# Performance work log

Measured on AMD Instinct MI355X. Metric: run time of the kernel, lower is better.

The kernel has to match this reference:

```python
import jax, jax.numpy as jnp
import numpy as np

N, E, G = 100000, 1600000, 64
FIN, D, OUT = 4, 64, 16
EPS = 1e-5


def _lin(key, fi, fo):
    kw, kb = jax.random.split(key)
    w = jax.random.normal(kw, (fi, fo), dtype=jnp.float32) / np.sqrt(fi)
    b = jnp.zeros((fo,), dtype=jnp.float32)
    return w, b


def setup_inputs() -> dict:
    key = jax.random.key(0)
    ks = jax.random.split(key, 24)
    inp = {}
    inp['h'] = jax.random.normal(ks[0], (N, FIN), dtype=jnp.float32)
    inp['pos'] = jax.random.normal(ks[1], (N, 3), dtype=jnp.float32)
    inp['edge_index'] = jax.random.randint(ks[2], (2, E), 0, N, dtype=jnp.int32)
    inp['batch'] = jnp.sort(jax.random.randint(ks[3], (N,), 0, G, dtype=jnp.int32))
    inp['fe_w'], inp['fe_b'] = _lin(ks[4], FIN, D)
    i = 5
    for c in ('c1', 'c2'):
        inp[c + 'h_w1'], inp[c + 'h_b1'] = _lin(ks[i], D, D); i += 1
        inp[c + 'h_w2'], inp[c + 'h_b2'] = _lin(ks[i], D, 3); i += 1
        inp[c + 'f_w1'], inp[c + 'f_b1'] = _lin(ks[i], D + 3, D); i += 1
        inp[c + 'f_w2'], inp[c + 'f_b2'] = _lin(ks[i], D, D); i += 1
        inp[c + 'g_w1'], inp[c + 'g_b1'] = _lin(ks[i], D, D); i += 1
        inp[c + 'g_gm'] = jnp.ones((D,), dtype=jnp.float32)
        inp[c + 'g_bt'] = jnp.zeros((D,), dtype=jnp.float32)
        inp[c + 'g_w2'], inp[c + 'g_b2'] = _lin(ks[i], D, D); i += 1
    inp['ro_w1'], inp['ro_b1'] = _lin(ks[i], D, D); i += 1
    inp['ro_w2'], inp['ro_b2'] = _lin(ks[i], D, OUT)
    return inp


def _mlp2(x, w1, b1, w2, b2):
    return jnp.maximum(x @ w1 + b1, 0.0) @ w2 + b2


def _bn(x, gm, bt):
    # BatchNorm1d in training mode: batch stats over the node axis
    m = jnp.mean(x, axis=0)
    v = jnp.var(x, axis=0)
    return (x - m) * jax.lax.rsqrt(v + EPS) * gm + bt


def _pointgnn_conv(x, pos, src, dst, hw1, hb1, hw2, hb2, fw1, fb1, fw2, fb2,
                   gw1, gb1, ggm, gbt, gw2, gb2):
    delta = _mlp2(x, hw1, hb1, hw2, hb2)                      # [N,3]
    rel = pos[src] - pos[dst] + delta[dst]                    # [E,3]
    msg = _mlp2(jnp.concatenate([rel, x[src]], axis=-1), fw1, fb1, fw2, fb2)  # [E,D]
    agg = jax.ops.segment_max(msg, dst, num_segments=x.shape[0])
    agg = jnp.where(jnp.isneginf(agg), 0.0, agg)              # empty segments -> 0
    g = jnp.maximum(agg @ gw1 + gb1, 0.0)
    g = _bn(g, ggm, gbt)
    return x + (g @ gw2 + gb2)


def reference(h, pos, edge_index, batch, fe_w, fe_b,
              c1h_w1, c1h_b1, c1h_w2, c1h_b2, c1f_w1, c1f_b1, c1f_w2, c1f_b2,
              c1g_w1, c1g_b1, c1g_gm, c1g_bt, c1g_w2, c1g_b2,
              c2h_w1, c2h_b1, c2h_w2, c2h_b2, c2f_w1, c2f_b1, c2f_w2, c2f_b2,
              c2g_w1, c2g_b1, c2g_gm, c2g_bt, c2g_w2, c2g_b2,
              ro_w1, ro_b1, ro_w2, ro_b2):
    src, dst = edge_index[0], edge_index[1]
    x = h @ fe_w + fe_b
    x = _pointgnn_conv(x, pos, src, dst, c1h_w1, c1h_b1, c1h_w2, c1h_b2,
                       c1f_w1, c1f_b1, c1f_w2, c1f_b2,
                       c1g_w1, c1g_b1, c1g_gm, c1g_bt, c1g_w2, c1g_b2)
    x = _pointgnn_conv(x, pos, src, dst, c2h_w1, c2h_b1, c2h_w2, c2h_b2,
                       c2f_w1, c2f_b1, c2f_w2, c2f_b2,
                       c2g_w1, c2g_b1, c2g_gm, c2g_bt, c2g_w2, c2g_b2)
    # global mean pool over graphs
    sums = jax.ops.segment_sum(x, batch, num_segments=G)
    cnts = jax.ops.segment_sum(jnp.ones((x.shape[0], 1), x.dtype), batch, num_segments=G)
    pooled = sums / jnp.maximum(cnts, 1.0)
    return _mlp2(pooled, ro_w1, ro_b1, ro_w2, ro_b2)
```

## Files before the change

kernel.cpp:

```cpp
#include <hip/hip_runtime.h>

#define NN 100000
#define NE 1600000
#define NG 64
#define EPS 1e-5f
#define SCAN_NB 98

#define FOR16(M) M(0) M(1) M(2) M(3) M(4) M(5) M(6) M(7) M(8) M(9) M(10) M(11) M(12) M(13) M(14) M(15)

#define WDECL(i) float4 wr##i##_;
#define LDW(i, RB, P) \
  wr##i##_.x = (P)[((RB) + 4 * i + 0) * 64 + lane]; \
  wr##i##_.y = (P)[((RB) + 4 * i + 1) * 64 + lane]; \
  wr##i##_.z = (P)[((RB) + 4 * i + 2) * 64 + lane]; \
  wr##i##_.w = (P)[((RB) + 4 * i + 3) * 64 + lane];
#define WPIN(i) asm volatile("" : "+v"(wr##i##_.x), "+v"(wr##i##_.y), "+v"(wr##i##_.z), "+v"(wr##i##_.w));
#define DOTR(i) { float4 v = xr[i]; \
  a0 = fmaf(v.x, wr##i##_.x, a0); a1 = fmaf(v.y, wr##i##_.y, a1); \
  a2 = fmaf(v.z, wr##i##_.z, a2); a3 = fmaf(v.w, wr##i##_.w, a3); }
#define DOTB(i, SRC) { \
  a0 = fmaf(bcast(SRC, 4 * i + 0), wr##i##_.x, a0); \
  a1 = fmaf(bcast(SRC, 4 * i + 1), wr##i##_.y, a1); \
  a2 = fmaf(bcast(SRC, 4 * i + 2), wr##i##_.z, a2); \
  a3 = fmaf(bcast(SRC, 4 * i + 3), wr##i##_.w, a3); }
#define DOTL(i) { float4 hv = hr[i]; \
  a0 = fmaf(hv.x, wr##i##_.x, a0); a1 = fmaf(hv.y, wr##i##_.y, a1); \
  a2 = fmaf(hv.z, wr##i##_.z, a2); a3 = fmaf(hv.w, wr##i##_.w, a3); }

#define BDECL(i) float4 br##i##_;
#define LDB(i, RB, P) \
  br##i##_.x = (P)[((RB) + 4 * i + 0) * 64 + lane]; \
  br##i##_.y = (P)[((RB) + 4 * i + 1) * 64 + lane]; \
  br##i##_.z = (P)[((RB) + 4 * i + 2) * 64 + lane]; \
  br##i##_.w = (P)[((RB) + 4 * i + 3) * 64 + lane];
#define BPIN(i) asm volatile("" : "+v"(br##i##_.x), "+v"(br##i##_.y), "+v"(br##i##_.z), "+v"(br##i##_.w));
#define DOTRB(i) { float4 v = xr[i]; \
  a0 = fmaf(v.x, br##i##_.x, a0); a1 = fmaf(v.y, br##i##_.y, a1); \
  a2 = fmaf(v.z, br##i##_.z, a2); a3 = fmaf(v.w, br##i##_.w, a3); }

__device__ __forceinline__ int wave_gid() {
  return __builtin_amdgcn_readfirstlane((int)((blockIdx.x * blockDim.x + threadIdx.x) >> 6));
}

__device__ __forceinline__ float bcast(float v, int l) {
  return __uint_as_float(__builtin_amdgcn_readlane(__float_as_uint(v), l));
}

__device__ __forceinline__ void graph_range(const int* __restrict__ batch, int g, int& s, int& e) {
  int a = 0, b = NN;
  while (a < b) { int m = (a + b) >> 1; if (batch[m] < g) a = m + 1; else b = m; }
  s = a;
  b = NN;
  while (a < b) { int m = (a + b) >> 1; if (batch[m] < g + 1) a = m + 1; else b = m; }
  e = a;
}

__global__ void k_zero(unsigned* __restrict__ hist, float* __restrict__ psum,
                       const float* __restrict__ pos, float4* __restrict__ pos4) {
  int i = blockIdx.x * blockDim.x + threadIdx.x;
  int st = gridDim.x * blockDim.x;
  for (int j = i; j < NN; j += st) {
    hist[j] = 0u;
    pos4[j] = make_float4(pos[(size_t)j * 3 + 0], pos[(size_t)j * 3 + 1],
                          pos[(size_t)j * 3 + 2], 0.f);
  }
  for (int j = i; j < NG * 64; j += st) psum[j] = 0.f;
}

__global__ void k_hist(const int* __restrict__ ei, unsigned* __restrict__ hist) {
  int i = blockIdx.x * blockDim.x + threadIdx.x;
  int st = gridDim.x * blockDim.x;
  for (int e = i; e < NE; e += st) atomicAdd(&hist[ei[NE + e]], 1u);
}

__global__ void k_scan1(const unsigned* __restrict__ hist, unsigned* __restrict__ coff,
                        unsigned* __restrict__ bsum) {
  __shared__ unsigned sd[256];
  int t = threadIdx.x;
  int base = blockIdx.x * 1024 + t * 4;
  unsigned v0 = (base + 0 < NN) ? hist[base + 0] : 0u;
  unsigned v1 = (base + 1 < NN) ? hist[base + 1] : 0u;
  unsigned v2 = (base + 2 < NN) ? hist[base + 2] : 0u;
  unsigned v3 = (base + 3 < NN) ? hist[base + 3] : 0u;
  unsigned tsum = v0 + v1 + v2 + v3;
  sd[t] = tsum;
  __syncthreads();
  for (int off = 1; off < 256; off <<= 1) {
    unsigned add = (t >= off) ? sd[t - off] : 0u;
    __syncthreads();
    sd[t] += add;
    __syncthreads();
  }
  unsigned p = sd[t] - tsum;
  if (t == 255) bsum[blockIdx.x] = sd[255];
  if (base + 0 < NN) coff[base + 0] = p; p += v0;
  if (base + 1 < NN) coff[base + 1] = p; p += v1;
  if (base + 2 < NN) coff[base + 2] = p; p += v2;
  if (base + 3 < NN) coff[base + 3] = p;
}

__global__ void k_scan2(unsigned* __restrict__ bsum) {
  __shared__ unsigned sd[128];
  int t = threadIdx.x;
  unsigned v = (t < SCAN_NB) ? bsum[t] : 0u;
  sd[t] = v;
  __syncthreads();
  for (int off = 1; off < 128; off <<= 1) {
    unsigned add = (t >= off) ? sd[t - off] : 0u;
    __syncthreads();
    sd[t] += add;
    __syncthreads();
  }
  if (t < SCAN_NB) bsum[t] = sd[t] - v;
}

__global__ void k_scan3(unsigned* __restrict__ coff, const unsigned* __restrict__ bsum,
                        unsigned* __restrict__ cursor) {
  int i = blockIdx.x * blockDim.x + threadIdx.x;
  if (i < NN) {
    unsigned v = coff[i] + bsum[i >> 10];
    coff[i] = v;
    cursor[i] = v;
  }
  if (i == 0) coff[NN] = NE;
}

__global__ void k_scatter(const int* __restrict__ ei, unsigned* __restrict__ cursor,
                          int* __restrict__ csrc) {
  int i = blockIdx.x * blockDim.x + threadIdx.x;
  int st = gridDim.x * blockDim.x;
  for (int e = i; e < NE; e += st) {
    int dst = ei[NE + e];
    unsigned p = atomicAdd(&cursor[dst], 1u);
    csrc[p] = ei[e];
  }
}

__global__ void __launch_bounds__(256) k_init_x(const float* __restrict__ h,
                                                const float* __restrict__ few,
                                                const float* __restrict__ feb,
                                                float* __restrict__ x) {
  int lane = threadIdx.x & 63;
  int wg = wave_gid();
  int nw = (gridDim.x * blockDim.x) >> 6;
  float c0 = few[0 * 64 + lane], c1 = few[1 * 64 + lane];
  float c2 = few[2 * 64 + lane], c3 = few[3 * 64 + lane];
  float b = feb[lane];
  for (int n = wg; n < NN; n += nw) {
    float4 hv = *(const float4*)(h + (size_t)n * 4);
    x[(size_t)n * 64 + lane] = fmaf(hv.x, c0, fmaf(hv.y, c1, fmaf(hv.z, c2, fmaf(hv.w, c3, b))));
  }
}

__global__ void __launch_bounds__(256) k_node_pre(
    const float* __restrict__ x, const float* __restrict__ pos,
    const float* __restrict__ hw1, const float* __restrict__ hb1,
    const float* __restrict__ hw2, const float* __restrict__ hb2,
    const float* __restrict__ fw1, const float* __restrict__ fb1,
    float* __restrict__ q, float* __restrict__ xa) {
  int lane = threadIdx.x & 63;
  int wg = wave_gid();
  int nw = (gridDim.x * blockDim.x) >> 6;
  FOR16(WDECL)
  FOR16(BDECL)
#define LD(i) LDW(i, 0, hw1)
  FOR16(LD)
#undef LD
#define LD(i) LDB(i, 3, fw1)
  FOR16(LD)
#undef LD
  FOR16(WPIN)
  FOR16(BPIN)
  float b1 = hb1[lane];
  float fb = fb1[lane];
  float u0 = hw2[lane * 3 + 0], u1 = hw2[lane * 3 + 1], u2 = hw2[lane * 3 + 2];
  float b20 = hb2[0], b21 = hb2[1], b22 = hb2[2];
  for (int n = wg; n < NN; n += nw) {
    const float4* xr = (const float4*)(x + (size_t)n * 64);
    float a0 = 0.f, a1 = 0.f, a2 = 0.f, a3 = 0.f;
    FOR16(DOTR)
    float t = fmaxf((a0 + a1) + (a2 + a3) + b1, 0.f);
    float p0 = t * u0, p1 = t * u1, p2 = t * u2;
#pragma unroll
    for (int off = 32; off; off >>= 1) {
      p0 += __shfl_xor(p0, off);
      p1 += __shfl_xor(p1, off);
      p2 += __shfl_xor(p2, off);
    }
    a0 = 0.f; a1 = 0.f; a2 = 0.f; a3 = 0.f;
    FOR16(DOTRB)
    xa[(size_t)n * 64 + lane] = (a0 + a1) + (a2 + a3) + fb;
    if (lane < 3) {
      float dc = (lane == 0) ? (p0 + b20) : ((lane == 1) ? (p1 + b21) : (p2 + b22));
      q[(size_t)n * 4 + lane] = pos[(size_t)n * 3 + lane] - dc;
    }
  }
}

__global__ void __launch_bounds__(256, 3) k_edge_csr(
    const float* __restrict__ xa, const float4* __restrict__ pos4,
    const float* __restrict__ q, const unsigned* __restrict__ coff,
    const int* __restrict__ csrc, const float* __restrict__ fw1,
    const float* __restrict__ fb2_, const float* __restrict__ fw2,
    float* __restrict__ agg) {
  __shared__ __align__(16) float hbuf[4][2][64];
  int lane = threadIdx.x & 63;
  int wid = threadIdx.x >> 6;
  int wg = wave_gid();
  int nw = (gridDim.x * blockDim.x) >> 6;
  FOR16(WDECL)
#define LD(i) LDW(i, 0, fw2)
  FOR16(LD)
#undef LD
  FOR16(WPIN)
  float pw0 = fw1[0 * 64 + lane], pw1 = fw1[1 * 64 + lane], pw2 = fw1[2 * 64 + lane];
  float bl = fb2_[lane];
  const float NEGINF = __int_as_float(0xff800000);
  for (int dst = wg; dst < NN; dst += nw) {
    unsigned s = coff[dst], e = coff[dst + 1];
    float mx;
    if (e > s) {
      float4 qd = *(const float4*)(q + (size_t)dst * 4);
      int src = csrc[s];
      float4 ps = pos4[src];
      float hh = xa[(size_t)src * 64 + lane];
      float pre = fmaxf(fmaf(ps.x - qd.x, pw0,
                        fmaf(ps.y - qd.y, pw1,
                        fmaf(ps.z - qd.z, pw2, hh))), 0.f);
      hbuf[wid][0][lane] = pre;
      int cur = 0;
      mx = NEGINF;
      for (unsigned i = s; i < e; ++i) {
        if (i + 1 < e) {
          int ns = csrc[i + 1];
          float4 ps2 = pos4[ns];
          float hh2 = xa[(size_t)ns * 64 + lane];
          float pre2 = fmaxf(fmaf(ps2.x - qd.x, pw0,
                             fmaf(ps2.y - qd.y, pw1,
                             fmaf(ps2.z - qd.z, pw2, hh2))), 0.f);
          hbuf[wid][cur ^ 1][lane] = pre2;
        }
        const float4* hr = (const float4*)hbuf[wid][cur];
        float a0 = bl, a1 = 0.f, a2 = 0.f, a3 = 0.f;
        DOTL(0) DOTL(1) DOTL(2) DOTL(3) DOTL(4) DOTL(5) DOTL(6) DOTL(7)
        __builtin_amdgcn_sched_barrier(0);
        DOTL(8) DOTL(9) DOTL(10) DOTL(11) DOTL(12) DOTL(13) DOTL(14) DOTL(15)
        mx = fmaxf(mx, (a0 + a1) + (a2 + a3));
        cur ^= 1;
      }
    } else {
      mx = 0.f;
    }
    agg[(size_t)dst * 64 + lane] = mx;
  }
}

__global__ void __launch_bounds__(256) k_g_bn(
    const float* __restrict__ agg, const float* __restrict__ gw1,
    const float* __restrict__ gb1, float* __restrict__ g, float* __restrict__ bnp) {
  __shared__ float2 red[4][64];
  int lane = threadIdx.x & 63;
  int wid = threadIdx.x >> 6;
  int wg = wave_gid();
  int nw = (gridDim.x * blockDim.x) >> 6;
  FOR16(WDECL)
#define LD(i) LDW(i, 0, gw1)
  FOR16(LD)
#undef LD
  FOR16(WPIN)
  float b = gb1[lane];
  float s = 0.f, ss = 0.f;
  for (int n = wg; n < NN; n += nw) {
    float av = agg[(size_t)n * 64 + lane];
    float a0 = 0.f, a1 = 0.f, a2 = 0.f, a3 = 0.f;
#define DB(i) DOTB(i, av)
    FOR16(DB)
#undef DB
    float gv = fmaxf((a0 + a1) + (a2 + a3) + b, 0.f);
    g[(size_t)n * 64 + lane] = gv;
    s += gv;
    ss += gv * gv;
  }
  red[wid][lane] = make_float2(s, ss);
  __syncthreads();
  if (wid == 0) {
    float2 r0 = red[0][lane], r1 = red[1][lane], r2 = red[2][lane], r3 = red[3][lane];
    bnp[(size_t)blockIdx.x * 128 + lane] = r0.x + r1.x + r2.x + r3.x;
    bnp[(size_t)blockIdx.x * 128 + 64 + lane] = r0.y + r1.y + r2.y + r3.y;
  }
}

#define NBLK_BN 256
__global__ void k_bn_final(const float* __restrict__ bnp, const float* __restrict__ gm,
                           const float* __restrict__ bt, const float* __restrict__ gw2,
                           const float* __restrict__ gb2, float* __restrict__ w2p,
                           float* __restrict__ b2p) {
  __shared__ float sums[128];
  __shared__ float sc[64], sh[64];
  int t = threadIdx.x;
  int c = t & 63;
  int kind = t >> 6;
  float acc = 0.f;
#pragma unroll 8
  for (int bId = 0; bId < NBLK_BN; ++bId) acc += bnp[(size_t)bId * 128 + kind * 64 + c];
  sums[t] = acc;
  __syncthreads();
  if (t < 64) {
    float mean = sums[t] * (1.f / (float)NN);
    float var = sums[64 + t] * (1.f / (float)NN) - mean * mean;
    float scale = gm[t] * rsqrtf(var + EPS);
    sc[t] = scale;
    sh[t] = bt[t] - mean * scale;
  }
  __syncthreads();
  for (int i = t; i < 4096; i += 128) {
    int d = i >> 6;
    w2p[i] = sc[d] * gw2[i];
  }
  if (t < 64) {
    float acc2 = gb2[t];
#pragma unroll 8
    for (int d = 0; d < 64; ++d) acc2 = fmaf(sh[d], gw2[d * 64 + t], acc2);
    b2p[t] = acc2;
  }
}

__global__ void __launch_bounds__(256) k_update(
    const float* __restrict__ g, const float* __restrict__ w2p,
    const float* __restrict__ b2p, float* __restrict__ x) {
  int lane = threadIdx.x & 63;
  int wg = wave_gid();
  int nw = (gridDim.x * blockDim.x) >> 6;
  FOR16(WDECL)
#define LD(i) LDW(i, 0, w2p)
  FOR16(LD)
#undef LD
  FOR16(WPIN)
  float b = b2p[lane];
  for (int n = wg; n < NN; n += nw) {
    const float4* xr = (const float4*)(g + (size_t)n * 64);
    float a0 = 0.f, a1 = 0.f, a2 = 0.f, a3 = 0.f;
    FOR16(DOTR)
    size_t idx = (size_t)n * 64 + lane;
    x[idx] = x[idx] + (a0 + a1) + (a2 + a3) + b;
  }
}

__global__ void __launch_bounds__(512) k_pool_partial(const float* __restrict__ x,
                                                      const int* __restrict__ batch,
                                                      float* __restrict__ psum) {
  __shared__ float red[8][64];
  int lane = threadIdx.x & 63;
  int wid = threadIdx.x >> 6;
  int g = blockIdx.x >> 2;
  int part = blockIdx.x & 3;
  int s, e;
  graph_range(batch, g, s, e);
  float acc = 0.f;
  for (int n = s + part * 8 + wid; n < e; n += 32) acc += x[(size_t)n * 64 + lane];
  red[wid][lane] = acc;
  __syncthreads();
  if (wid == 0) {
    float t = acc;
#pragma unroll
    for (int w = 1; w < 8; ++w) t += red[w][lane];
    atomicAdd(&psum[(size_t)g * 64 + lane], t);
  }
}

__global__ void __launch_bounds__(64) k_readout(
    const float* __restrict__ psum, const int* __restrict__ batch,
    const float* __restrict__ w1, const float* __restrict__ b1,
    const float* __restrict__ w2, const float* __restrict__ b2,
    float* __restrict__ out) {
  __shared__ float hs[64];
  int lane = threadIdx.x;
  int g = blockIdx.x;
  int s, e;
  graph_range(batch, g, s, e);
  float scale = 1.f / fmaxf((float)(e - s), 1.f);
  FOR16(WDECL)
#define LD(i) LDW(i, 0, w1)
  FOR16(LD)
#undef LD
  const float4* xr = (const float4*)(psum + (size_t)g * 64);
  float a0 = 0.f, a1 = 0.f, a2 = 0.f, a3 = 0.f;
  FOR16(DOTR)
  hs[lane] = fmaxf(((a0 + a1) + (a2 + a3)) * scale + b1[lane], 0.f);
  __syncthreads();
  if (lane < 16) {
    float acc = b2[lane];
#pragma unroll
    for (int l = 0; l < 64; ++l) acc = fmaf(hs[l], w2[l * 16 + lane], acc);
    out[(size_t)g * 16 + lane] = acc;
  }
}

extern "C" void kernel_launch(void* const* d_in, const int* in_sizes, int n_in,
                              void* d_out, int out_size, void* d_ws, size_t ws_size,
                              hipStream_t stream) {
  const float* h = (const float*)d_in[0];
  const float* pos = (const float*)d_in[1];
  const int* ei = (const int*)d_in[2];
  const int* batch = (const int*)d_in[3];
  const float* fe_w = (const float*)d_in[4];
  const float* fe_b = (const float*)d_in[5];
  const float* ro_w1 = (const float*)d_in[34];
  const float* ro_b1 = (const float*)d_in[35];
  const float* ro_w2 = (const float*)d_in[36];
  const float* ro_b2 = (const float*)d_in[37];
  float* out = (float*)d_out;

  char* ws = (char*)d_ws;
  const size_t SZ_ROW = (size_t)NN * 64 * sizeof(float);
  float* x = (float*)(ws); ws += SZ_ROW;
  float* xa = (float*)(ws); ws += SZ_ROW;
  float* agg = (float*)(ws); ws += SZ_ROW;
  float* q = (float*)(ws); ws += (size_t)NN * 4 * sizeof(float);
  float* bnp = (float*)(ws); ws += (size_t)NBLK_BN * 128 * sizeof(float);
  float* w2p = (float*)(ws); ws += 4096 * sizeof(float);
  float* b2p = (float*)(ws); ws += 256;
  float* psum = (float*)(ws); ws += (size_t)NG * 64 * sizeof(float);
  float4* pos4 = (float4*)(ws); ws += (size_t)NN * sizeof(float4);
  unsigned* cursor = (unsigned*)(ws); ws += ((size_t)NN * 4 + 256);
  unsigned* coff = (unsigned*)(ws); ws += ((size_t)(NN + 1) * 4 + 252);
  unsigned* bsum = (unsigned*)(ws); ws += 512;
  int* csrc = (int*)(ws); ws += (size_t)NE * 4;

  const int NB_NODE = 512;
  const int NB_EDGE = 4096;

  k_zero<<<256, 256, 0, stream>>>(cursor, psum, pos, pos4);
  k_hist<<<1024, 256, 0, stream>>>(ei, cursor);
  k_scan1<<<SCAN_NB, 256, 0, stream>>>(cursor, coff, bsum);
  k_scan2<<<1, 128, 0, stream>>>(bsum);
  k_scan3<<<392, 256, 0, stream>>>(coff, bsum, cursor);
  k_scatter<<<1024, 256, 0, stream>>>(ei, cursor, csrc);

  k_init_x<<<NB_NODE, 256, 0, stream>>>(h, fe_w, fe_b, x);

  for (int layer = 0; layer < 2; ++layer) {
    int base = (layer == 0) ? 6 : 20;
    const float* hw1 = (const float*)d_in[base + 0];
    const float* hb1 = (const float*)d_in[base + 1];
    const float* hw2 = (const float*)d_in[base + 2];
    const float* hb2 = (const float*)d_in[base + 3];
    const float* fw1 = (const float*)d_in[base + 4];
    const float* fb1 = (const float*)d_in[base + 5];
    const float* fw2 = (const float*)d_in[base + 6];
    const float* fb2 = (const float*)d_in[base + 7];
    const float* gw1 = (const float*)d_in[base + 8];
    const float* gb1 = (const float*)d_in[base + 9];
    const float* ggm = (const float*)d_in[base + 10];
    const float* gbt = (const float*)d_in[base + 11];
    const float* gw2 = (const float*)d_in[base + 12];
    const float* gb2 = (const float*)d_in[base + 13];

    k_node_pre<<<NB_NODE, 256, 0, stream>>>(x, pos, hw1, hb1, hw2, hb2, fw1, fb1, q, xa);
    k_edge_csr<<<NB_EDGE, 256, 0, stream>>>(xa, pos4, q, coff, csrc, fw1, fb2, fw2, agg);
    float* g = xa;
    k_g_bn<<<NBLK_BN, 256, 0, stream>>>(agg, gw1, gb1, g, bnp);
    k_bn_final<<<1, 128, 0, stream>>>(bnp, ggm, gbt, gw2, gb2, w2p, b2p);
    k_update<<<NB_NODE, 256, 0, stream>>>(g, w2p, b2p, x);
  }

  k_pool_partial<<<NG * 4, 512, 0, stream>>>(x, batch, psum);
  k_readout<<<NG, 64, 0, stream>>>(psum, batch, ro_w1, ro_b1, ro_w2, ro_b2, out);
}
```

Before: 1.434 ms.

## Use packed FMA with readlane broadcast in edge and g kernels

The edge kernel no longer stages the per-edge hidden vector in LDS double buffers. It now computes it in registers and broadcasts each element across lanes with readlane. Dot products in both the edge and g/BN kernels switch to two-wide packed FMAs (v_pk_fma_f32) on float2 accumulators, and the occupancy hint of 3 is dropped from the edge kernel's launch bounds. This removes LDS traffic and aims to double FMA throughput, but relies on 64 scalar readlanes per edge, which may serialize on the SALU/VALU path.

```diff
diff --git a/kernel.cpp b/kernel.cpp
--- a/kernel.cpp
+++ b/kernel.cpp
@@ -5,6 +5,8 @@
 #define NG 64
 #define EPS 1e-5f
 #define SCAN_NB 98
+
+typedef float v2f __attribute__((ext_vector_type(2)));
 
 #define FOR16(M) M(0) M(1) M(2) M(3) M(4) M(5) M(6) M(7) M(8) M(9) M(10) M(11) M(12) M(13) M(14) M(15)
 
@@ -18,14 +20,13 @@
 #define DOTR(i) { float4 v = xr[i]; \
   a0 = fmaf(v.x, wr##i##_.x, a0); a1 = fmaf(v.y, wr##i##_.y, a1); \
   a2 = fmaf(v.z, wr##i##_.z, a2); a3 = fmaf(v.w, wr##i##_.w, a3); }
-#define DOTB(i, SRC) { \
-  a0 = fmaf(bcast(SRC, 4 * i + 0), wr##i##_.x, a0); \
-  a1 = fmaf(bcast(SRC, 4 * i + 1), wr##i##_.y, a1); \
-  a2 = fmaf(bcast(SRC, 4 * i + 2), wr##i##_.z, a2); \
-  a3 = fmaf(bcast(SRC, 4 * i + 3), wr##i##_.w, a3); }
-#define DOTL(i) { float4 hv = hr[i]; \
-  a0 = fmaf(hv.x, wr##i##_.x, a0); a1 = fmaf(hv.y, wr##i##_.y, a1); \
-  a2 = fmaf(hv.z, wr##i##_.z, a2); a3 = fmaf(hv.w, wr##i##_.w, a3); }
+#define DOTB2(i, SRC) { \
+  v2f bc0 = { bcast(SRC, 4 * i + 0), bcast(SRC, 4 * i + 1) }; \
+  v2f bc1 = { bcast(SRC, 4 * i + 2), bcast(SRC, 4 * i + 3) }; \
+  v2f w0 = { wr##i##_.x, wr##i##_.y }; \
+  v2f w1 = { wr##i##_.z, wr##i##_.w }; \
+  ac01 = bc0 * w0 + ac01; \
+  ac23 = bc1 * w1 + ac23; }
 
 #define BDECL(i) float4 br##i##_;
 #define LDB(i, RB, P) \
@@ -197,15 +198,13 @@
   }
 }
 
-__global__ void __launch_bounds__(256, 3) k_edge_csr(
+__global__ void __launch_bounds__(256) k_edge_csr(
     const float* __restrict__ xa, const float4* __restrict__ pos4,
     const float* __restrict__ q, const unsigned* __restrict__ coff,
     const int* __restrict__ csrc, const float* __restrict__ fw1,
     const float* __restrict__ fb2_, const float* __restrict__ fw2,
     float* __restrict__ agg) {
-  __shared__ __align__(16) float hbuf[4][2][64];
-  int lane = threadIdx.x & 63;
-  int wid = threadIdx.x >> 6;
+  int lane = threadIdx.x & 63;
   int wg = wave_gid();
   int nw = (gridDim.x * blockDim.x) >> 6;
   FOR16(WDECL)
@@ -224,29 +223,23 @@
       int src = csrc[s];
       float4 ps = pos4[src];
       float hh = xa[(size_t)src * 64 + lane];
-      float pre = fmaxf(fmaf(ps.x - qd.x, pw0,
-                        fmaf(ps.y - qd.y, pw1,
-                        fmaf(ps.z - qd.z, pw2, hh))), 0.f);
-      hbuf[wid][0][lane] = pre;
-      int cur = 0;
       mx = NEGINF;
       for (unsigned i = s; i < e; ++i) {
+        float4 cps = ps;
+        float chh = hh;
         if (i + 1 < e) {
           int ns = csrc[i + 1];
-          float4 ps2 = pos4[ns];
-          float hh2 = xa[(size_t)ns * 64 + lane];
-          float pre2 = fmaxf(fmaf(ps2.x - qd.x, pw0,
-                             fmaf(ps2.y - qd.y, pw1,
-                             fmaf(ps2.z - qd.z, pw2, hh2))), 0.f);
-          hbuf[wid][cur ^ 1][lane] = pre2;
+          ps = pos4[ns];
+          hh = xa[(size_t)ns * 64 + lane];
         }
-        const float4* hr = (const float4*)hbuf[wid][cur];
-        float a0 = bl, a1 = 0.f, a2 = 0.f, a3 = 0.f;
-        DOTL(0) DOTL(1) DOTL(2) DOTL(3) DOTL(4) DOTL(5) DOTL(6) DOTL(7)
-        __builtin_amdgcn_sched_barrier(0);
-        DOTL(8) DOTL(9) DOTL(10) DOTL(11) DOTL(12) DOTL(13) DOTL(14) DOTL(15)
-        mx = fmaxf(mx, (a0 + a1) + (a2 + a3));
-        cur ^= 1;
+        float pre = fmaxf(fmaf(cps.x - qd.x, pw0,
+                          fmaf(cps.y - qd.y, pw1,
+                          fmaf(cps.z - qd.z, pw2, chh))), 0.f);
+        v2f ac01 = {0.f, 0.f}, ac23 = {0.f, 0.f};
+#define DB(i) DOTB2(i, pre)
+        FOR16(DB)
+#undef DB
+        mx = fmaxf(mx, (ac01.x + ac01.y) + (ac23.x + ac23.y) + bl);
       }
     } else {
       mx = 0.f;
@@ -272,11 +265,11 @@
   float s = 0.f, ss = 0.f;
   for (int n = wg; n < NN; n += nw) {
     float av = agg[(size_t)n * 64 + lane];
-    float a0 = 0.f, a1 = 0.f, a2 = 0.f, a3 = 0.f;
-#define DB(i) DOTB(i, av)
+    v2f ac01 = {0.f, 0.f}, ac23 = {0.f, 0.f};
+#define DB(i) DOTB2(i, av)
     FOR16(DB)
 #undef DB
-    float gv = fmaxf((a0 + a1) + (a2 + a3) + b, 0.f);
+    float gv = fmaxf((ac01.x + ac01.y) + (ac23.x + ac23.y) + b, 0.f);
     g[(size_t)n * 64 + lane] = gv;
     s += gv;
     ss += gv * gv;
```

Result: faster. 1.381 ms (-3.7%).
